# Optimization experiments

Hardware: AMD Instinct MI355X
Metric: run time of the kernel (lower is better)

## Reference

```python
import jax, jax.numpy as jnp
import numpy as np

N, FIN, F, H = 4096, 128, 64, 8
NEG = -1e10


def setup_inputs() -> dict:
    key = jax.random.key(0)
    ks = jax.random.split(key, 6)
    X = jax.random.normal(ks[0], (N, FIN), dtype=jnp.float32)
    # sparse-ish binary adjacency with self loops, stored dense (as the layer expects)
    A = (jax.random.uniform(ks[1], (N, N)) < 0.05).astype(jnp.int32)
    A = A.at[jnp.arange(N), jnp.arange(N)].set(1)
    W = jax.random.normal(ks[2], (H, FIN, F), dtype=jnp.float32) * (1.0 / np.sqrt(FIN))
    b = jnp.zeros((H, F), dtype=jnp.float32)
    a_self = jax.random.normal(ks[3], (H, F), dtype=jnp.float32) * (1.0 / np.sqrt(F))
    a_neigh = jax.random.normal(ks[4], (H, F), dtype=jnp.float32) * (1.0 / np.sqrt(F))
    return {"X": X, "A": A, "W": W, "b": b, "a_self": a_self, "a_neigh": a_neigh}


def reference(X, A, W, b, a_self, a_neigh):
    # Dropout layers run in inference mode in the original call -> identity.
    feats = jnp.einsum('nf,hfo->hno', X, W)              # [H, N, F]
    s_self = jnp.einsum('hno,ho->hn', feats, a_self)     # [H, N]
    s_neigh = jnp.einsum('hno,ho->hn', feats, a_neigh)   # [H, N]
    scores = s_self[:, :, None] + s_neigh[:, None, :]    # [H, N, N]
    scores = jnp.where(scores > 0, scores, 0.2 * scores)  # LeakyReLU(0.2)
    mask = (1.0 - A.astype(jnp.float32)) * NEG            # [N, N]
    attn = jax.nn.softmax(scores + mask[None], axis=-1)   # [H, N, N]
    out = jnp.einsum('hnm,hmo->hno', attn, feats) + b[:, None, :]
    out = jax.nn.elu(out)                                 # [H, N, F]
    # concat heads -> [N, H*F]
    return jnp.transpose(out, (1, 0, 2)).reshape(N, H * F)
```

## Files before the change

kernel.cpp:

```cpp
#include <hip/hip_runtime.h>
#include <cmath>


#define NN 4096
#define FIN 128
#define FF 64
#define HH 8

typedef _Float16 h2 __attribute__((ext_vector_type(2)));
typedef _Float16 h4 __attribute__((ext_vector_type(4)));
typedef _Float16 h8 __attribute__((ext_vector_type(8)));
typedef float f32x2 __attribute__((ext_vector_type(2)));
typedef float f32x4 __attribute__((ext_vector_type(4)));

union H8 {
  h8 v;
  h2 p[4];
};
union U2 {
  h2 h;
  unsigned u;
};

static __device__ __forceinline__ float dot2acc(h2 a, float c) {
#if __has_builtin(__builtin_amdgcn_fdot2)
  return __builtin_amdgcn_fdot2(a, (h2){(_Float16)1.f, (_Float16)1.f}, c,
                                false);
#else
  return c + (float)a[0] + (float)a[1];
#endif
}

static __device__ __forceinline__ unsigned mask2(unsigned w, int j) {
#if __has_builtin(__builtin_amdgcn_sbfe) && __has_builtin(__builtin_amdgcn_perm)
  int lo = __builtin_amdgcn_sbfe((int)w, j, 1);
  int hi = __builtin_amdgcn_sbfe((int)w, j + 1, 1);
  return __builtin_amdgcn_perm((unsigned)hi, (unsigned)lo, 0x05040100u);
#else
  int lo = ((int)(w << (31 - j))) >> 31;
  int hi = ((int)(w << (30 - j))) >> 31;
  return ((unsigned)lo & 0xFFFFu) | ((unsigned)hi << 16);
#endif
}

static __device__ __forceinline__ void gload16(const void* g, void* l) {
  __builtin_amdgcn_global_load_lds(
      (const __attribute__((address_space(1))) unsigned int*)g,
      (__attribute__((address_space(3))) unsigned int*)l, 16, 0, 0);
}

__global__ __launch_bounds__(256) void pack_kernel(
    const int* __restrict__ A, const float* __restrict__ W,
    const float* __restrict__ X, unsigned long long* __restrict__ bits,
    _Float16* __restrict__ Wsw, _Float16* __restrict__ Xsw) {
  const int b = blockIdx.x;
  const int tid = threadIdx.x;
  const int wave = tid >> 6, lane = tid & 63;
  if (b < NN) {
    __shared__ int ldsT[4][4][256];
    const int* ar = A + (size_t)b * NN;
    int4 v[4];
#pragma unroll
    for (int it = 0; it < 4; ++it) {
      const int g = wave * 4 + it;
      v[it] = *(const int4*)(ar + g * 256 + lane * 4);
    }
#pragma unroll
    for (int it = 0; it < 4; ++it) *(int4*)&ldsT[wave][it][lane * 4] = v[it];
    unsigned long long* br = bits + ((size_t)b << 6);
#pragma unroll
    for (int it = 0; it < 4; ++it) {
      const int g = wave * 4 + it;
      int w0 = ldsT[wave][it][0 * 64 + lane];
      int w1 = ldsT[wave][it][1 * 64 + lane];
      int w2 = ldsT[wave][it][2 * 64 + lane];
      int w3 = ldsT[wave][it][3 * 64 + lane];
      unsigned long long m0 = __ballot(w0 != 0);
      unsigned long long m1 = __ballot(w1 != 0);
      unsigned long long m2 = __ballot(w2 != 0);
      unsigned long long m3 = __ballot(w3 != 0);
      if (lane == 0) {
        ulonglong2 p0 = {m0, m1}, p1 = {m2, m3};
        *(ulonglong2*)(br + g * 4 + 0) = p0;
        *(ulonglong2*)(br + g * 4 + 2) = p1;
      }
    }
  } else if (b < NN + 2) {
    const int h0 = (b - NN) * 4;
    for (int h = h0; h < h0 + 4; ++h) {
      for (int c = tid; c < 1024; c += 256) {
        int ln = c & 63, nb = (c >> 6) & 3, kt = c >> 8;
        int f = nb * 16 + (ln & 15);
        int k0 = kt * 32 + (ln >> 4) * 8;
        h8 v;
#pragma unroll
        for (int j = 0; j < 8; ++j)
          v[j] = (_Float16)W[((size_t)(h * FIN) + k0 + j) * FF + f];
        *(h8*)(Wsw + ((size_t)(((h * 4 + kt) * 4 + nb) * 64 + ln)) * 8) = v;
      }
    }
  } else {
    const int tile = (b - NN - 2) * 4 + wave;
    const int l16 = lane & 15, quad = lane >> 4;
    const float* xr = X + (size_t)(tile * 16 + l16) * FIN;
#pragma unroll
    for (int kt = 0; kt < 4; ++kt) {
      int k0 = kt * 32 + quad * 8;
      f32x4 x0 = *(const f32x4*)(xr + k0);
      f32x4 x1 = *(const f32x4*)(xr + k0 + 4);
      h8 v = {(_Float16)x0[0], (_Float16)x0[1], (_Float16)x0[2],
              (_Float16)x0[3], (_Float16)x1[0], (_Float16)x1[1],
              (_Float16)x1[2], (_Float16)x1[3]};
      *(h8*)(Xsw + ((size_t)((tile * 4 + kt) * 64 + lane)) * 8) = v;
    }
  }
}

__global__ __launch_bounds__(256) void feats_kernel(
    const _Float16* __restrict__ Xsw, const _Float16* __restrict__ Wsw,
    const float* __restrict__ a_self, const float* __restrict__ a_neigh,
    _Float16* __restrict__ feats_sw, _Float16* __restrict__ es_h,
    _Float16* __restrict__ esn_h, _Float16* __restrict__ et_h,
    _Float16* __restrict__ etn_h) {
  const int h = blockIdx.y;
  const int tid = threadIdx.x, wave = tid >> 6, lane = tid & 63;
  const int l16 = lane & 15, quad = lane >> 4;
  const int rt = blockIdx.x * 4 + wave;
  const int r0 = rt * 16;

  f32x4 acc[4];
#pragma unroll
  for (int nb = 0; nb < 4; ++nb) acc[nb] = (f32x4){0.f, 0.f, 0.f, 0.f};

  const _Float16* xp = Xsw + ((size_t)(rt * 4) * 64 + lane) * 8;
  const _Float16* wp = Wsw + ((size_t)(h * 16) * 64 + lane) * 8;
  h8 Af[4];
#pragma unroll
  for (int kt = 0; kt < 4; ++kt) Af[kt] = *(const h8*)(xp + kt * 512);
#pragma unroll
  for (int kt = 0; kt < 4; ++kt)
#pragma unroll
    for (int nb = 0; nb < 4; ++nb) {
      h8 Bf = *(const h8*)(wp + (kt * 4 + nb) * 512);
      acc[nb] = __builtin_amdgcn_mfma_f32_16x16x32_f16(Af[kt], Bf, acc[nb], 0, 0, 0);
    }

  float as[4], an[4];
#pragma unroll
  for (int nb = 0; nb < 4; ++nb) {
    as[nb] = a_self[h * FF + nb * 16 + l16];
    an[nb] = a_neigh[h * FF + nb * 16 + l16];
  }
#pragma unroll
  for (int r = 0; r < 4; ++r) {
    float ps = acc[0][r] * as[0] + acc[1][r] * as[1] + acc[2][r] * as[2] +
               acc[3][r] * as[3];
    float pn = acc[0][r] * an[0] + acc[1][r] * an[1] + acc[2][r] * an[2] +
               acc[3][r] * an[3];
#pragma unroll
    for (int m = 1; m <= 8; m <<= 1) {
      ps += __shfl_xor(ps, m, 64);
      pn += __shfl_xor(pn, m, 64);
    }
    if (l16 == 0) {
      int node = h * NN + r0 + quad * 4 + r;
      es_h[node] = (_Float16)__expf(ps - 2.0f);
      esn_h[node] = (_Float16)__expf(0.2f * ps - 2.0f);
      et_h[node] = (_Float16)__expf(pn - 2.0f);
      etn_h[node] = (_Float16)__expf(0.2f * pn - 2.0f);
    }
  }

  const int kb = r0 >> 5;
  const int quadA = ((r0 >> 4) & 1) * 2 + (quad >> 1);
  const int jbase = (quad & 1) << 2;
#pragma unroll
  for (int nb = 0; nb < 4; ++nb) {
    h4 v = {(_Float16)acc[nb][0], (_Float16)acc[nb][1], (_Float16)acc[nb][2],
            (_Float16)acc[nb][3]};
    size_t off = ((size_t)((h * 128 + kb) * 4 + nb) << 9) +
                 ((quadA * 16 + l16) << 3) + jbase;
    *(h4*)(feats_sw + off) = v;
  }
}

__global__ __launch_bounds__(512, 2) void attn_kernel(
    const unsigned long long* __restrict__ Abits,
    const _Float16* __restrict__ feats_sw, const _Float16* __restrict__ es_h,
    const _Float16* __restrict__ esn_h, const _Float16* __restrict__ et_h,
    const _Float16* __restrict__ etn_h, const float* __restrict__ bias,
    float* __restrict__ out) {
  const int bid = blockIdx.x;
  const int h = bid & 7, n0 = (bid >> 3) << 7;
  const int tid = threadIdx.x, wave = tid >> 6, lane = tid & 63;
  const int l16 = lane & 15, quad = lane >> 4;
  const int shq = quad << 3;

  __shared__ __align__(16) char smem[3 * 20480];

  const int myrow = n0 + (wave << 4) + l16;
  _Float16 e = es_h[h * NN + myrow];
  _Float16 en = esn_h[h * NN + myrow];
  const h2 esp = (h2){e, e};
  const h2 esnp = (h2){en, en};

  f32x4 acc[4];
#pragma unroll
  for (int nb = 0; nb < 4; ++nb) acc[nb] = (f32x4){0.f, 0.f, 0.f, 0.f};
  float dsA = 0.f, dsB = 0.f;

  const char* gF = (const char*)feats_sw + ((size_t)h << 19);
  const char* gE = (const char*)et_h + (h << 13);
  const char* gEN = (const char*)etn_h + (h << 13);
  const char* gB = (const char*)Abits + ((size_t)n0 << 9);

#define STAGE(s_, bw_)                                                        \
  do {                                                                        \
    char* L_ = smem + (bw_)*20480;                                            \
    const char* src_ = gF + ((size_t)(s_) << 14) + (wave << 11) + (lane << 4);\
    gload16(src_, L_ + (wave << 11) + (lane << 4));                           \
    gload16(src_ + 1024, L_ + (wave << 11) + 1024 + (lane << 4));             \
    if (wave == 0)                                                            \
      gload16(gE + ((s_) << 8) + (l16 << 4), L_ + 16384 + (lane << 4));       \
    if (wave == 1)                                                            \
      gload16(gEN + ((s_) << 8) + (l16 << 4), L_ + 17408 + (lane << 4));      \
    if (wave == 2)                                                            \
      gload16(gB + ((size_t)lane << 9) + ((s_) << 4),                         \
              L_ + 18432 + (lane << 4));                                      \
    if (wave == 3)                                                            \
      gload16(gB + ((size_t)(64 + lane) << 9) + ((s_) << 4),                  \
              L_ + 18432 + 1024 + (lane << 4));                               \
  } while (0)

  STAGE(0, 0);
  STAGE(1, 1);

  for (int s = 0; s < 32; ++s) {
    const int bC = s % 3;
    if (s < 30) {
      STAGE(s + 2, (s + 2) % 3);
      __builtin_amdgcn_sched_barrier(0);
      if (wave < 4)
        asm volatile("s_waitcnt vmcnt(6)" ::: "memory");
      else
        asm volatile("s_waitcnt vmcnt(4)" ::: "memory");
    } else if (s == 30) {
      __builtin_amdgcn_sched_barrier(0);
      if (wave < 4)
        asm volatile("s_waitcnt vmcnt(3)" ::: "memory");
      else
        asm volatile("s_waitcnt vmcnt(2)" ::: "memory");
    } else {
      __builtin_amdgcn_sched_barrier(0);
      asm volatile("s_waitcnt vmcnt(0)" ::: "memory");
    }
    __builtin_amdgcn_sched_barrier(0);
    __builtin_amdgcn_s_barrier();

    const char* L = smem + bC * 20480;
#pragma unroll
    for (int c = 0; c < 2; ++c) {
      unsigned long long myb = *(const unsigned long long*)(
          L + 18432 + (((wave << 4) + l16) << 4) + (c << 3));
#pragma unroll
      for (int kf = 0; kf < 2; ++kf) {
        H8 ET, ETN;
        ET.v = *(const h8*)(L + 16384 + (c << 7) + (kf << 6) + (quad << 4));
        ETN.v = *(const h8*)(L + 17408 + (c << 7) + (kf << 6) + (quad << 4));
        const char* fB = L + (c << 13) + (kf << 12) + (lane << 4);
        h8 B0 = *(const h8*)(fB);
        h8 B1 = *(const h8*)(fB + 1024);
        h8 B2 = *(const h8*)(fB + 2048);
        h8 B3 = *(const h8*)(fB + 3072);
        unsigned wsw = (unsigned)(myb >> (kf ? 32 : 0)) >> shq;
        H8 P;
#pragma unroll
        for (int p = 0; p < 4; ++p) {
          h2 a_ = esp * ET.p[p];
          h2 b_ = esnp * ETN.p[p];
          h2 r_ = __builtin_elementwise_max(a_, b_);
          U2 u_;
          u_.h = r_;
          u_.u &= mask2(wsw, 2 * p);
          P.p[p] = u_.h;
          if (p & 1)
            dsB = dot2acc(u_.h, dsB);
          else
            dsA = dot2acc(u_.h, dsA);
        }
        acc[0] = __builtin_amdgcn_mfma_f32_16x16x32_f16(P.v, B0, acc[0], 0, 0, 0);
        acc[1] = __builtin_amdgcn_mfma_f32_16x16x32_f16(P.v, B1, acc[1], 0, 0, 0);
        acc[2] = __builtin_amdgcn_mfma_f32_16x16x32_f16(P.v, B2, acc[2], 0, 0, 0);
        acc[3] = __builtin_amdgcn_mfma_f32_16x16x32_f16(P.v, B3, acc[3], 0, 0, 0);
      }
    }
  }
#undef STAGE

  float den = dsA + dsB;
  den += __shfl_xor(den, 16, 64);
  den += __shfl_xor(den, 32, 64);
  const int orow = n0 + (wave << 4) + (quad << 2);
#pragma unroll
  for (int r = 0; r < 4; ++r) {
    float dr = __shfl(den, (quad << 2) + r, 64);
    float inv = 1.0f / dr;
#pragma unroll
    for (int nb = 0; nb < 4; ++nb) {
      float x = acc[nb][r] * inv + bias[h * FF + nb * 16 + l16];
      x = x > 0.f ? x : (__expf(x) - 1.0f);
      out[(size_t)(orow + r) * (HH * FF) + h * FF + nb * 16 + l16] = x;
    }
  }
}

extern "C" void kernel_launch(void* const* d_in, const int* in_sizes, int n_in,
                              void* d_out, int out_size, void* d_ws,
                              size_t ws_size, hipStream_t stream) {
  const float* X = (const float*)d_in[0];
  const int* A = (const int*)d_in[1];
  const float* W = (const float*)d_in[2];
  const float* b = (const float*)d_in[3];
  const float* a_self = (const float*)d_in[4];
  const float* a_neigh = (const float*)d_in[5];
  float* out = (float*)d_out;

  char* ws = (char*)d_ws;
  unsigned long long* Abits = (unsigned long long*)ws;
  _Float16* feats_sw = (_Float16*)(ws + (2u << 20));
  _Float16* es_h = (_Float16*)(ws + (6u << 20));
  _Float16* esn_h = (_Float16*)(ws + (6u << 20) + (64u << 10));
  _Float16* et_h = (_Float16*)(ws + (6u << 20) + (128u << 10));
  _Float16* etn_h = (_Float16*)(ws + (6u << 20) + (192u << 10));
  _Float16* Wsw = (_Float16*)(ws + (6u << 20) + (256u << 10));
  _Float16* Xsw = (_Float16*)(ws + (6u << 20) + (384u << 10));

  pack_kernel<<<NN + 66, 256, 0, stream>>>(A, W, X, Abits, Wsw, Xsw);
  feats_kernel<<<dim3(64, 8), 256, 0, stream>>>(Xsw, Wsw, a_self, a_neigh,
                                                feats_sw, es_h, esn_h, et_h,
                                                etn_h);
  attn_kernel<<<256, 512, 0, stream>>>(Abits, feats_sw, es_h, esn_h, et_h,
                                       etn_h, b, out);
}
```

Baseline: 146.0 us.

## Split attention K-chunks across wave halves and halve rows per block

Each attention block now covers 64 rows instead of 128, so the grid doubles to 512 blocks. Waves 0-3 and 4-7 each handle one half of every 64-column K chunk for the same 16-row tiles. The partial accumulators and denominators are then reduced through shared memory before the ELU epilogue. The aim is more blocks for the 256 CUs, a higher occupancy target and a barrier moved ahead of the next stage load so the triple-buffered pipeline is simpler. The cost is that each block reloads the full feats stream for half the rows, which doubles global/L2 traffic for feats, and adds a shared-memory reduction at the end.

```diff
diff --git a/kernel.cpp b/kernel.cpp
--- a/kernel.cpp
+++ b/kernel.cpp
@@ -184,21 +184,22 @@
   }
 }
 
-__global__ __launch_bounds__(512, 2) void attn_kernel(
+__global__ __launch_bounds__(512, 4) void attn_kernel(
     const unsigned long long* __restrict__ Abits,
     const _Float16* __restrict__ feats_sw, const _Float16* __restrict__ es_h,
     const _Float16* __restrict__ esn_h, const _Float16* __restrict__ et_h,
     const _Float16* __restrict__ etn_h, const float* __restrict__ bias,
     float* __restrict__ out) {
   const int bid = blockIdx.x;
-  const int h = bid & 7, n0 = (bid >> 3) << 7;
+  const int h = bid & 7, n0 = (bid >> 3) << 6;
   const int tid = threadIdx.x, wave = tid >> 6, lane = tid & 63;
   const int l16 = lane & 15, quad = lane >> 4;
   const int shq = quad << 3;
-
-  __shared__ __align__(16) char smem[3 * 20480];
-
-  const int myrow = n0 + (wave << 4) + l16;
+  const int rtile = wave & 3, half = wave >> 2;
+
+  __shared__ __align__(16) char smem[3 * 19456];
+
+  const int myrow = n0 + (rtile << 4) + l16;
   _Float16 e = es_h[h * NN + myrow];
   _Float16 en = esn_h[h * NN + myrow];
   const h2 esp = (h2){e, e};
@@ -214,85 +215,70 @@
   const char* gEN = (const char*)etn_h + (h << 13);
   const char* gB = (const char*)Abits + ((size_t)n0 << 9);
 
-#define STAGE(s_, bw_)                                                        \
-  do {                                                                        \
-    char* L_ = smem + (bw_)*20480;                                            \
-    const char* src_ = gF + ((size_t)(s_) << 14) + (wave << 11) + (lane << 4);\
-    gload16(src_, L_ + (wave << 11) + (lane << 4));                           \
-    gload16(src_ + 1024, L_ + (wave << 11) + 1024 + (lane << 4));             \
-    if (wave == 0)                                                            \
-      gload16(gE + ((s_) << 8) + (l16 << 4), L_ + 16384 + (lane << 4));       \
-    if (wave == 1)                                                            \
-      gload16(gEN + ((s_) << 8) + (l16 << 4), L_ + 17408 + (lane << 4));      \
-    if (wave == 2)                                                            \
-      gload16(gB + ((size_t)lane << 9) + ((s_) << 4),                         \
-              L_ + 18432 + (lane << 4));                                      \
-    if (wave == 3)                                                            \
-      gload16(gB + ((size_t)(64 + lane) << 9) + ((s_) << 4),                  \
-              L_ + 18432 + 1024 + (lane << 4));                               \
+#define STAGE(s_, bw_)                                                         \
+  do {                                                                         \
+    char* L_ = smem + (bw_)*19456;                                             \
+    const char* src_ = gF + ((size_t)(s_) << 14) + (wave << 11) + (lane << 4); \
+    gload16(src_, L_ + (wave << 11) + (lane << 4));                            \
+    gload16(src_ + 1024, L_ + (wave << 11) + 1024 + (lane << 4));              \
+    if (wave == 0)                                                             \
+      gload16(gE + ((s_) << 8) + (l16 << 4), L_ + 16384 + (lane << 4));        \
+    if (wave == 1)                                                             \
+      gload16(gEN + ((s_) << 8) + (l16 << 4), L_ + 17408 + (lane << 4));       \
+    if (wave == 2)                                                             \
+      gload16(gB + ((size_t)lane << 9) + ((s_) << 4), L_ + 18432 + (lane << 4)); \
   } while (0)
 
   STAGE(0, 0);
   STAGE(1, 1);
 
   for (int s = 0; s < 32; ++s) {
-    const int bC = s % 3;
-    if (s < 30) {
-      STAGE(s + 2, (s + 2) % 3);
-      __builtin_amdgcn_sched_barrier(0);
-      if (wave < 4)
-        asm volatile("s_waitcnt vmcnt(6)" ::: "memory");
-      else
-        asm volatile("s_waitcnt vmcnt(4)" ::: "memory");
-    } else if (s == 30) {
-      __builtin_amdgcn_sched_barrier(0);
-      if (wave < 4)
+    __builtin_amdgcn_sched_barrier(0);
+    if (s < 31) {
+      if (wave < 3)
         asm volatile("s_waitcnt vmcnt(3)" ::: "memory");
       else
         asm volatile("s_waitcnt vmcnt(2)" ::: "memory");
     } else {
-      __builtin_amdgcn_sched_barrier(0);
       asm volatile("s_waitcnt vmcnt(0)" ::: "memory");
     }
     __builtin_amdgcn_sched_barrier(0);
     __builtin_amdgcn_s_barrier();
-
-    const char* L = smem + bC * 20480;
-#pragma unroll
-    for (int c = 0; c < 2; ++c) {
-      unsigned long long myb = *(const unsigned long long*)(
-          L + 18432 + (((wave << 4) + l16) << 4) + (c << 3));
-#pragma unroll
-      for (int kf = 0; kf < 2; ++kf) {
-        H8 ET, ETN;
-        ET.v = *(const h8*)(L + 16384 + (c << 7) + (kf << 6) + (quad << 4));
-        ETN.v = *(const h8*)(L + 17408 + (c << 7) + (kf << 6) + (quad << 4));
-        const char* fB = L + (c << 13) + (kf << 12) + (lane << 4);
-        h8 B0 = *(const h8*)(fB);
-        h8 B1 = *(const h8*)(fB + 1024);
-        h8 B2 = *(const h8*)(fB + 2048);
-        h8 B3 = *(const h8*)(fB + 3072);
-        unsigned wsw = (unsigned)(myb >> (kf ? 32 : 0)) >> shq;
-        H8 P;
-#pragma unroll
-        for (int p = 0; p < 4; ++p) {
-          h2 a_ = esp * ET.p[p];
-          h2 b_ = esnp * ETN.p[p];
-          h2 r_ = __builtin_elementwise_max(a_, b_);
-          U2 u_;
-          u_.h = r_;
-          u_.u &= mask2(wsw, 2 * p);
-          P.p[p] = u_.h;
-          if (p & 1)
-            dsB = dot2acc(u_.h, dsB);
-          else
-            dsA = dot2acc(u_.h, dsA);
-        }
-        acc[0] = __builtin_amdgcn_mfma_f32_16x16x32_f16(P.v, B0, acc[0], 0, 0, 0);
-        acc[1] = __builtin_amdgcn_mfma_f32_16x16x32_f16(P.v, B1, acc[1], 0, 0, 0);
-        acc[2] = __builtin_amdgcn_mfma_f32_16x16x32_f16(P.v, B2, acc[2], 0, 0, 0);
-        acc[3] = __builtin_amdgcn_mfma_f32_16x16x32_f16(P.v, B3, acc[3], 0, 0, 0);
+    if (s < 30) STAGE(s + 2, (s + 2) % 3);
+
+    const char* L = smem + (s % 3) * 19456;
+    unsigned long long myb = *(const unsigned long long*)(
+        L + 18432 + (((rtile << 4) + l16) << 4) + (half << 3));
+#pragma unroll
+    for (int kf = 0; kf < 2; ++kf) {
+      H8 ET, ETN;
+      ET.v = *(const h8*)(L + 16384 + (half << 7) + (kf << 6) + (quad << 4));
+      ETN.v = *(const h8*)(L + 17408 + (half << 7) + (kf << 6) + (quad << 4));
+      const char* fB = L + (half << 13) + (kf << 12) + (lane << 4);
+      h8 B0 = *(const h8*)(fB);
+      h8 B1 = *(const h8*)(fB + 1024);
+      h8 B2 = *(const h8*)(fB + 2048);
+      h8 B3 = *(const h8*)(fB + 3072);
+      unsigned wsw = (unsigned)(myb >> (kf ? 32 : 0)) >> shq;
+      H8 P;
+#pragma unroll
+      for (int p = 0; p < 4; ++p) {
+        h2 a_ = esp * ET.p[p];
+        h2 b_ = esnp * ETN.p[p];
+        h2 r_ = __builtin_elementwise_max(a_, b_);
+        U2 u_;
+        u_.h = r_;
+        u_.u &= mask2(wsw, 2 * p);
+        P.p[p] = u_.h;
+        if (p & 1)
+          dsB = dot2acc(u_.h, dsB);
+        else
+          dsA = dot2acc(u_.h, dsA);
       }
+      acc[0] = __builtin_amdgcn_mfma_f32_16x16x32_f16(P.v, B0, acc[0], 0, 0, 0);
+      acc[1] = __builtin_amdgcn_mfma_f32_16x16x32_f16(P.v, B1, acc[1], 0, 0, 0);
+      acc[2] = __builtin_amdgcn_mfma_f32_16x16x32_f16(P.v, B2, acc[2], 0, 0, 0);
+      acc[3] = __builtin_amdgcn_mfma_f32_16x16x32_f16(P.v, B3, acc[3], 0, 0, 0);
     }
   }
 #undef STAGE
@@ -300,16 +286,33 @@
   float den = dsA + dsB;
   den += __shfl_xor(den, 16, 64);
   den += __shfl_xor(den, 32, 64);
-  const int orow = n0 + (wave << 4) + (quad << 2);
-#pragma unroll
-  for (int r = 0; r < 4; ++r) {
-    float dr = __shfl(den, (quad << 2) + r, 64);
-    float inv = 1.0f / dr;
-#pragma unroll
-    for (int nb = 0; nb < 4; ++nb) {
-      float x = acc[nb][r] * inv + bias[h * FF + nb * 16 + l16];
-      x = x > 0.f ? x : (__expf(x) - 1.0f);
-      out[(size_t)(orow + r) * (HH * FF) + h * FF + nb * 16 + l16] = x;
+
+  float(*accL)[16][68] = (float(*)[16][68])smem;
+  float(*denL)[16] = (float(*)[16])(smem + 4 * 16 * 68 * 4);
+  __syncthreads();
+  if (half == 1) {
+#pragma unroll
+    for (int nb = 0; nb < 4; ++nb)
+#pragma unroll
+      for (int r = 0; r < 4; ++r)
+        accL[rtile][quad * 4 + r][nb * 16 + l16] = acc[nb][r];
+    if (quad == 0) denL[rtile][l16] = den;
+  }
+  __syncthreads();
+  if (half == 0) {
+    float dtot = den + denL[rtile][l16];
+    const int orow = n0 + (rtile << 4) + (quad << 2);
+#pragma unroll
+    for (int r = 0; r < 4; ++r) {
+      float dr = __shfl(dtot, (quad << 2) + r, 64);
+      float inv = 1.0f / dr;
+#pragma unroll
+      for (int nb = 0; nb < 4; ++nb) {
+        float x = (acc[nb][r] + accL[rtile][quad * 4 + r][nb * 16 + l16]) * inv +
+                  bias[h * FF + nb * 16 + l16];
+        x = x > 0.f ? x : (__expf(x) - 1.0f);
+        out[(size_t)(orow + r) * (HH * FF) + h * FF + nb * 16 + l16] = x;
+      }
     }
   }
 }
@@ -339,6 +342,6 @@
   feats_kernel<<<dim3(64, 8), 256, 0, stream>>>(Xsw, Wsw, a_self, a_neigh,
                                                 feats_sw, es_h, esn_h, et_h,
                                                 etn_h);
-  attn_kernel<<<256, 512, 0, stream>>>(Abits, feats_sw, es_h, esn_h, et_h,
+  attn_kernel<<<512, 512, 0, stream>>>(Abits, feats_sw, es_h, esn_h, et_h,
                                        etn_h, b, out);
 }
```

Result: no change. 144.8 us (-0.8%).
